# Performance work log

Measured on AMD Instinct MI355X. Metric: run time of the kernel, lower is better.

## Reference

```python
import jax, jax.numpy as jnp
import numpy as np

B, S, H, NH = 4, 1024, 1024, 16
HD = H // NH
I = 4096
EPS = 1e-12
BASE = 10000.0


def setup_inputs() -> dict:
    key = jax.random.key(0)
    ks = jax.random.split(key, 6)
    sc = 0.02
    return {
        "x": jax.random.normal(ks[0], (B, S, H), jnp.float32),
        "ln1_w": jnp.ones((H,), jnp.float32),
        "ln1_b": jnp.zeros((H,), jnp.float32),
        "qkv_w": jax.random.normal(ks[1], (3 * H, H), jnp.float32) * sc,
        "qkv_b": jnp.zeros((3 * H,), jnp.float32),
        "out_w": jax.random.normal(ks[2], (H, H), jnp.float32) * sc,
        "out_b": jnp.zeros((H,), jnp.float32),
        "ln2_w": jnp.ones((H,), jnp.float32),
        "ln2_b": jnp.zeros((H,), jnp.float32),
        "i2h_w": jax.random.normal(ks[3], (2 * I, H), jnp.float32) * sc,
        "i2h_b": jnp.zeros((2 * I,), jnp.float32),
        "h2o_w": jax.random.normal(ks[4], (H, I), jnp.float32) * sc,
        "h2o_b": jnp.zeros((H,), jnp.float32),
    }


def _layer_norm(x, w, b, eps=EPS):
    mu = jnp.mean(x, axis=-1, keepdims=True)
    var = jnp.mean(jnp.square(x - mu), axis=-1, keepdims=True)
    return (x - mu) * jax.lax.rsqrt(var + eps) * w + b


def _rope_cos_sin(seq_len, dim, base):
    # inv_freq = base ** linspace(0, -1 + 2/dim, dim//2), repeated twice
    half = jnp.power(base, jnp.linspace(0.0, -1.0 + 2.0 / dim, dim // 2, dtype=jnp.float32))
    inv_freq = jnp.concatenate([half, half])  # [dim]
    t = jnp.arange(seq_len, dtype=jnp.float32)
    freqs = t[:, None] * inv_freq[None, :]  # [seq, dim]
    return jnp.cos(freqs), jnp.sin(freqs)


def _rotate(x, cos, sin):
    # x: [B, NH, S, HD]; cos/sin: [S, HD]
    xl, xr = jnp.split(x, 2, axis=-1)
    x_rot = jnp.concatenate([-xr, xl], axis=-1)
    return x * cos + x_rot * sin


def _forward(x, ln1_w, ln1_b, qkv_w, qkv_b, out_w, out_b,
             ln2_w, ln2_b, i2h_w, i2h_b, h2o_w, h2o_b):
    b, s, h = x.shape
    # --- LeanSelfAttention (pre-LN, rotary, causal, residual) ---
    h_ln = _layer_norm(x, ln1_w, ln1_b)
    qkv = h_ln @ qkv_w.T + qkv_b  # [b, s, 3h]
    q, k, v = jnp.split(qkv, 3, axis=-1)
    to_heads = lambda t: t.reshape(b, s, NH, HD).transpose(0, 2, 1, 3)  # [b,nh,s,hd]
    q, k, v = to_heads(q), to_heads(k), to_heads(v)
    cos, sin = _rope_cos_sin(s, HD, BASE)
    q, k = _rotate(q, cos, sin), _rotate(k, cos, sin)
    scores = jnp.einsum("bhqd,bhkd->bhqk", q, k) / np.sqrt(HD).astype(np.float32)
    causal = jnp.tril(jnp.ones((s, s), dtype=bool))
    scores = jnp.where(causal, scores, jnp.float32(-10000.0))
    probs = jax.nn.softmax(scores, axis=-1)
    attn = jnp.einsum("bhqk,bhkd->bhqd", probs, v)
    attn = attn.transpose(0, 2, 1, 3).reshape(b, s, h)
    attn_out = attn @ out_w.T + out_b + x  # residual
    # --- LeanFFN (pre-LN, gated gelu, residual) ---
    ffn_ln = _layer_norm(attn_out, ln2_w, ln2_b)
    pre = ffn_ln @ i2h_w.T + i2h_b  # [b, s, 2I]
    gate, lin = jnp.split(pre, 2, axis=-1)
    hid = jax.nn.gelu(gate, approximate=False) * lin
    return hid @ h2o_w.T + h2o_b + attn_out


def reference(x, ln1_w, ln1_b, qkv_w, qkv_b, out_w, out_b,
              ln2_w, ln2_b, i2h_w, i2h_b, h2o_w, h2o_b):
    return _forward(x, ln1_w, ln1_b, qkv_w, qkv_b, out_w, out_b,
                    ln2_w, ln2_b, i2h_w, i2h_b, h2o_w, h2o_b)
```

## Files before the change

### kernel.cpp

```cpp
#include <hip/hip_runtime.h>
#include <cstdint>
#include <cstddef>

typedef __bf16 bf16;
typedef __bf16 bf16x4 __attribute__((ext_vector_type(4)));
typedef __bf16 bf16x8 __attribute__((ext_vector_type(8)));
typedef float  f32x4  __attribute__((ext_vector_type(4)));

#define GLD16(gptr, lptr)                                                      \
  __builtin_amdgcn_global_load_lds(                                            \
      (__attribute__((address_space(1))) unsigned int*)(gptr),                 \
      (__attribute__((address_space(3))) unsigned int*)(lptr), 16, 0, 0)

__global__ __launch_bounds__(256)
void convert_kernel(const float* __restrict__ src, bf16* __restrict__ dst, int n8)
{
    const int j = blockIdx.x * 256 + threadIdx.x;
    if (j >= n8) return;
    const float* s = src + (size_t)j * 8;
    bf16x8 o;
#pragma unroll
    for (int e = 0; e < 8; ++e) o[e] = (bf16)s[e];
    ((bf16x8*)dst)[j] = o;
}

template<class InT>
__global__ __launch_bounds__(256)
void ln_kernel(const InT* __restrict__ x, const float* __restrict__ w,
               const float* __restrict__ b, bf16* __restrict__ out)
{
    __shared__ float red[8];
    const int row = blockIdx.x;
    const int tid = threadIdx.x;
    const InT* xr = x + (size_t)row * 1024;
    float xf[4], s = 0.f, ss = 0.f;
#pragma unroll
    for (int j = 0; j < 4; ++j) {
        xf[j] = (float)xr[tid * 4 + j];
        s += xf[j]; ss += xf[j] * xf[j];
    }
#pragma unroll
    for (int off = 32; off > 0; off >>= 1) { s += __shfl_xor(s, off); ss += __shfl_xor(ss, off); }
    if ((tid & 63) == 0) { red[(tid >> 6) * 2] = s; red[(tid >> 6) * 2 + 1] = ss; }
    __syncthreads();
    s  = red[0] + red[2] + red[4] + red[6];
    ss = red[1] + red[3] + red[5] + red[7];
    const float mu   = s * (1.f / 1024.f);
    const float var  = ss * (1.f / 1024.f) - mu * mu;
    const float rstd = rsqrtf(var + 1e-12f);
    bf16x4 ov;
#pragma unroll
    for (int j = 0; j < 4; ++j)
        ov[j] = (bf16)((xf[j] - mu) * rstd * w[tid * 4 + j] + b[tid * 4 + j]);
    *(bf16x4*)(out + (size_t)row * 1024 + tid * 4) = ov;
}

template<int RES_MODE, bool OUT_F32>
__global__ __launch_bounds__(256)
void gemm_bt(const bf16* __restrict__ A, const bf16* __restrict__ W,
             const float* __restrict__ bias, const void* __restrict__ res,
             void* __restrict__ Cv, int M, int N, int K)
{
    __shared__ alignas(16) bf16 As[128][32];
    __shared__ alignas(16) bf16 Bs[128][32];
    const int tid  = threadIdx.x;
    const int lane = tid & 63, wid = tid >> 6;
    const int lr = lane & 15, lg = lane >> 4;
    const int kgrp = lg * 8;
    const int wm = (wid >> 1) * 64, wn = (wid & 1) * 64;
    const int row0 = blockIdx.x * 128, col0 = blockIdx.y * 128;

    f32x4 acc[4][4] = {};

    for (int k0 = 0; k0 < K; k0 += 32) {
#pragma unroll
        for (int i = 0; i < 2; ++i) {
            const int c = i * 256 + tid;
            const int r = c >> 2, k8 = (c & 3) * 8;
            GLD16(A + (size_t)(row0 + r) * K + k0 + k8,
                  (char*)&As[0][0] + (size_t)(i * 256 + wid * 64) * 16);
            GLD16(W + (size_t)(col0 + r) * K + k0 + k8,
                  (char*)&Bs[0][0] + (size_t)(i * 256 + wid * 64) * 16);
        }
        __syncthreads();
        bf16x8 af[4], bw[4];
#pragma unroll
        for (int mi = 0; mi < 4; ++mi) af[mi] = *(const bf16x8*)&As[wm + mi * 16 + lr][kgrp];
#pragma unroll
        for (int ni = 0; ni < 4; ++ni) bw[ni] = *(const bf16x8*)&Bs[wn + ni * 16 + lr][kgrp];
#pragma unroll
        for (int mi = 0; mi < 4; ++mi)
#pragma unroll
            for (int ni = 0; ni < 4; ++ni)
                acc[mi][ni] = __builtin_amdgcn_mfma_f32_16x16x32_bf16(
                    af[mi], bw[ni], acc[mi][ni], 0, 0, 0);
        __syncthreads();
    }

#pragma unroll
    for (int ni = 0; ni < 4; ++ni) {
        const int ccol = col0 + wn + ni * 16 + lr;
        const float bv = bias[ccol];
#pragma unroll
        for (int mi = 0; mi < 4; ++mi)
#pragma unroll
            for (int r = 0; r < 4; ++r) {
                const size_t crow = (size_t)(row0 + wm + mi * 16 + lg * 4 + r);
                float v = acc[mi][ni][r] + bv;
                if constexpr (RES_MODE == 1) v += ((const float*)res)[crow * N + ccol];
                if constexpr (RES_MODE == 2) v += (float)((const bf16*)res)[crow * N + ccol];
                if constexpr (OUT_F32) ((float*)Cv)[crow * N + ccol] = v;
                else                   ((bf16*)Cv)[crow * N + ccol] = (bf16)v;
            }
    }
}

__global__ __launch_bounds__(256)
void gemm_h2o_sk(const bf16* __restrict__ A, const bf16* __restrict__ W,
                 float* __restrict__ part)
{
    __shared__ alignas(16) bf16 As[128][32];
    __shared__ alignas(16) bf16 Bs[128][32];
    const int tid  = threadIdx.x;
    const int lane = tid & 63, wid = tid >> 6;
    const int lr = lane & 15, lg = lane >> 4;
    const int kgrp = lg * 8;
    const int wm = (wid >> 1) * 64, wn = (wid & 1) * 64;
    const int row0 = blockIdx.x * 128, col0 = blockIdx.y * 128;
    const int kbase = blockIdx.z * 1024;
    const int K = 4096;

    f32x4 acc[4][4] = {};

    for (int k0 = kbase; k0 < kbase + 1024; k0 += 32) {
#pragma unroll
        for (int i = 0; i < 2; ++i) {
            const int c = i * 256 + tid;
            const int r = c >> 2, k8 = (c & 3) * 8;
            GLD16(A + (size_t)(row0 + r) * K + k0 + k8,
                  (char*)&As[0][0] + (size_t)(i * 256 + wid * 64) * 16);
            GLD16(W + (size_t)(col0 + r) * K + k0 + k8,
                  (char*)&Bs[0][0] + (size_t)(i * 256 + wid * 64) * 16);
        }
        __syncthreads();
        bf16x8 af[4], bw[4];
#pragma unroll
        for (int mi = 0; mi < 4; ++mi) af[mi] = *(const bf16x8*)&As[wm + mi * 16 + lr][kgrp];
#pragma unroll
        for (int ni = 0; ni < 4; ++ni) bw[ni] = *(const bf16x8*)&Bs[wn + ni * 16 + lr][kgrp];
#pragma unroll
        for (int mi = 0; mi < 4; ++mi)
#pragma unroll
            for (int ni = 0; ni < 4; ++ni)
                acc[mi][ni] = __builtin_amdgcn_mfma_f32_16x16x32_bf16(
                    af[mi], bw[ni], acc[mi][ni], 0, 0, 0);
        __syncthreads();
    }

    float* dst = part + (size_t)blockIdx.z * 4096 * 1024;
#pragma unroll
    for (int ni = 0; ni < 4; ++ni) {
        const int ccol = col0 + wn + ni * 16 + lr;
#pragma unroll
        for (int mi = 0; mi < 4; ++mi)
#pragma unroll
            for (int r = 0; r < 4; ++r) {
                const size_t crow = (size_t)(row0 + wm + mi * 16 + lg * 4 + r);
                dst[crow * 1024 + ccol] = acc[mi][ni][r];
            }
    }
}

__global__ __launch_bounds__(256)
void h2o_reduce(const float* __restrict__ part, const float* __restrict__ bias,
                const bf16* __restrict__ res, float* __restrict__ out)
{
    const size_t g = ((size_t)blockIdx.x * 256 + threadIdx.x) * 4;
    const int col = (int)(g & 1023);
    f32x4 v = *(const f32x4*)(part + g);
#pragma unroll
    for (int s = 1; s < 4; ++s) {
        const f32x4 p = *(const f32x4*)(part + (size_t)s * 4096 * 1024 + g);
#pragma unroll
        for (int j = 0; j < 4; ++j) v[j] += p[j];
    }
    const f32x4 bv = *(const f32x4*)(bias + col);
    const bf16x4 rv = *(const bf16x4*)(res + g);
    f32x4 o;
#pragma unroll
    for (int j = 0; j < 4; ++j) o[j] = v[j] + bv[j] + (float)rv[j];
    *(f32x4*)(out + g) = o;
}

__global__ __launch_bounds__(256)
void gemm_qkv_rope(const bf16* __restrict__ A, const bf16* __restrict__ W,
                   const float* __restrict__ bias, bf16* __restrict__ q_r,
                   bf16* __restrict__ k_r, bf16* __restrict__ v_r)
{
    __shared__ alignas(16) bf16 As[128][32];
    __shared__ alignas(16) bf16 Bs[128][32];
    const int tid  = threadIdx.x;
    const int lane = tid & 63, wid = tid >> 6;
    const int lr = lane & 15, lg = lane >> 4;
    const int kgrp = lg * 8;
    const int wm = (wid >> 1) * 64, wn = (wid & 1) * 64;
    const int row0 = blockIdx.x * 128, col0 = blockIdx.y * 128;
    const int K = 1024;

    f32x4 acc[4][4] = {};

    for (int k0 = 0; k0 < K; k0 += 32) {
#pragma unroll
        for (int i = 0; i < 2; ++i) {
            const int c = i * 256 + tid;
            const int r = c >> 2, k8 = (c & 3) * 8;
            GLD16(A + (size_t)(row0 + r) * K + k0 + k8,
                  (char*)&As[0][0] + (size_t)(i * 256 + wid * 64) * 16);
            GLD16(W + (size_t)(col0 + r) * K + k0 + k8,
                  (char*)&Bs[0][0] + (size_t)(i * 256 + wid * 64) * 16);
        }
        __syncthreads();
        bf16x8 af[4], bw[4];
#pragma unroll
        for (int mi = 0; mi < 4; ++mi) af[mi] = *(const bf16x8*)&As[wm + mi * 16 + lr][kgrp];
#pragma unroll
        for (int ni = 0; ni < 4; ++ni) bw[ni] = *(const bf16x8*)&Bs[wn + ni * 16 + lr][kgrp];
#pragma unroll
        for (int mi = 0; mi < 4; ++mi)
#pragma unroll
            for (int ni = 0; ni < 4; ++ni)
                acc[mi][ni] = __builtin_amdgcn_mfma_f32_16x16x32_bf16(
                    af[mi], bw[ni], acc[mi][ni], 0, 0, 0);
        __syncthreads();
    }

    const int third = blockIdx.y >> 3;
    bf16* dst = (third == 0) ? q_r : (third == 1) ? k_r : v_r;
    const float qs = (third == 0) ? 0.125f : 1.f;
#pragma unroll
    for (int ni = 0; ni < 2; ++ni) {
        const int i_ = ni * 16 + lr;
        const int ccol = col0 + wn + ni * 16 + lr;
        const int h = (ccol >> 6) & 15;
        const float blo = bias[ccol], bhi = bias[ccol + 32];
        const float inv = __expf((float)i_ * (-9.210340371976184f / 32.f));
#pragma unroll
        for (int mi = 0; mi < 4; ++mi)
#pragma unroll
            for (int r = 0; r < 4; ++r) {
                const int crow = row0 + wm + mi * 16 + lg * 4 + r;
                const int s = crow & 1023, b = crow >> 10;
                const float lo = acc[mi][ni][r] + blo;
                const float hi = acc[mi][ni + 2][r] + bhi;
                const size_t ob = ((size_t)(b * 16 + h) * 1024 + s) * 64;
                if (third == 2) {
                    dst[ob + i_]      = (bf16)lo;
                    dst[ob + i_ + 32] = (bf16)hi;
                } else {
                    float sn, c;
                    sincosf((float)s * inv, &sn, &c);
                    dst[ob + i_]      = (bf16)((lo * c - hi * sn) * qs);
                    dst[ob + i_ + 32] = (bf16)((hi * c + lo * sn) * qs);
                }
            }
    }
}

__global__ __launch_bounds__(512, 2)
void gemm_i2h_g8(const bf16* __restrict__ A, const bf16* __restrict__ W,
                 const float* __restrict__ bias, bf16* __restrict__ hid)
{
    __shared__ alignas(16) char smem[3 * 32768];
    const int tid  = threadIdx.x;
    const int lane = tid & 63, wid = tid >> 6;
    const int lrr  = lane & 15, lg = lane >> 4;
    const int wr = wid >> 2, wc = wid & 3;
    const int row0 = blockIdx.x * 256;
    const int colh = blockIdx.y * 128 + wc * 32;
    const int NT = 32;

    const int cA0 = tid, cA1 = 512 + tid;
    const int rA0 = cA0 >> 2, rA1 = cA1 >> 2, rB = tid >> 2;
    const int swA0 = (((cA0 & 3) * 16) ^ (((rA0 >> 1) & 3) << 4)) >> 1;
    const int swA1 = (((cA1 & 3) * 16) ^ (((rA1 >> 1) & 3) << 4)) >> 1;
    const int swB  = (((tid & 3) * 16) ^ (((rB  >> 1) & 3) << 4)) >> 1;
    const bf16* gA0 = A + (size_t)(row0 + rA0) * 1024 + swA0;
    const bf16* gA1 = A + (size_t)(row0 + rA1) * 1024 + swA1;
    const bf16* gBg = W + (size_t)(blockIdx.y * 128 + rB) * 1024 + swB;
    const bf16* gBl = W + (size_t)(4096 + blockIdx.y * 128 + rB) * 1024 + swB;
    const int dA0 = (wid * 64) * 16, dA1 = (512 + wid * 64) * 16, dB = (wid * 64) * 16;

    f32x4 acc[8][4] = {};

    {
        char* b0 = smem;
        GLD16(gBg, b0 + 16384 + dB); GLD16(gBl, b0 + 24576 + dB);
        GLD16(gA0, b0 + dA0);        GLD16(gA1, b0 + dA1);
        char* b1 = smem + 32768;
        GLD16(gBg + 32, b1 + 16384 + dB); GLD16(gBl + 32, b1 + 24576 + dB);
        GLD16(gA0 + 32, b1 + dA0);        GLD16(gA1 + 32, b1 + dA1);
    }
    asm volatile("s_waitcnt vmcnt(4)\ns_barrier" ::: "memory");

    int cur = 0, stg = 2;
    for (int t = 0; t < NT; ++t) {
        const char* bA  = smem + cur * 32768;
        const char* bBg = bA + 16384;
        const char* bBl = bA + 24576;
        char* sB = smem + stg * 32768;
        const int k0s = (t + 2) * 32;
        const bool dostg = (t < NT - 2);

        if (dostg) { GLD16(gBg + k0s, sB + 16384 + dB); GLD16(gBl + k0s, sB + 24576 + dB); }
        bf16x8 bf[4], af[4];
        const int bcol = lg * 16;
#pragma unroll
        for (int nv = 0; nv < 4; ++nv) {
            const int row = wc * 32 + (nv & 1) * 16 + lrr;
            const char* base = (nv < 2) ? bBg : bBl;
            bf[nv] = *(const bf16x8*)(base + row * 64 + (bcol ^ (((row >> 1) & 3) << 4)));
        }
#pragma unroll
        for (int mi = 0; mi < 4; ++mi) {
            const int row = wr * 128 + mi * 16 + lrr;
            af[mi] = *(const bf16x8*)(bA + row * 64 + (bcol ^ (((row >> 1) & 3) << 4)));
        }
        __builtin_amdgcn_s_barrier();
        __builtin_amdgcn_s_setprio(1);
#pragma unroll
        for (int mi = 0; mi < 4; ++mi)
#pragma unroll
            for (int nv = 0; nv < 4; ++nv)
                acc[mi][nv] = __builtin_amdgcn_mfma_f32_16x16x32_bf16(
                    af[mi], bf[nv], acc[mi][nv], 0, 0, 0);
        __builtin_amdgcn_s_setprio(0);
        __builtin_amdgcn_s_barrier();

        if (dostg) { GLD16(gA0 + k0s, sB + dA0); GLD16(gA1 + k0s, sB + dA1); }
#pragma unroll
        for (int mi = 0; mi < 4; ++mi) {
            const int row = wr * 128 + (4 + mi) * 16 + lrr;
            af[mi] = *(const bf16x8*)(bA + row * 64 + (bcol ^ (((row >> 1) & 3) << 4)));
        }
        __builtin_amdgcn_s_barrier();
        __builtin_amdgcn_s_setprio(1);
#pragma unroll
        for (int mi = 0; mi < 4; ++mi)
#pragma unroll
            for (int nv = 0; nv < 4; ++nv)
                acc[4 + mi][nv] = __builtin_amdgcn_mfma_f32_16x16x32_bf16(
                    af[mi], bf[nv], acc[4 + mi][nv], 0, 0, 0);
        __builtin_amdgcn_s_setprio(0);

        if (dostg) asm volatile("s_waitcnt vmcnt(4)\ns_barrier" ::: "memory");
        else       asm volatile("s_waitcnt vmcnt(0)\ns_barrier" ::: "memory");
        cur = (cur == 2) ? 0 : cur + 1;
        stg = (stg == 2) ? 0 : stg + 1;
    }

#pragma unroll
    for (int c = 0; c < 2; ++c) {
        const int gcol = colh + c * 16 + lrr;
        const float bg_ = bias[gcol], bl_ = bias[4096 + gcol];
#pragma unroll
        for (int mi = 0; mi < 8; ++mi)
#pragma unroll
            for (int r = 0; r < 4; ++r) {
                const size_t row = (size_t)(row0 + wr * 128 + mi * 16 + lg * 4 + r);
                const float g = acc[mi][c][r] + bg_;
                const float l = acc[mi][2 + c][r] + bl_;
                const float ge = 0.5f * g * (1.f + erff(g * 0.70710678118654752f));
                hid[row * 4096 + gcol] = (bf16)(ge * l);
            }
    }
}

__global__ __launch_bounds__(256)
void attn_kernel(const bf16* __restrict__ q_r, const bf16* __restrict__ k_r,
                 const bf16* __restrict__ v_r, bf16* __restrict__ attn)
{
    __shared__ alignas(16) bf16 Ks[64][72];
    __shared__ alignas(16) bf16 Vt[64][72];
    __shared__ alignas(16) bf16 Ps[4][16][72];
    const int qt = blockIdx.x, bh = blockIdx.y;
    const int tid = threadIdx.x, lane = tid & 63, w = tid >> 6;
    const int lr = lane & 15, lg = lane >> 4;
    const int kgrp = lg * 8;
    const int qbase = qt * 64;

    const bf16* qrow = q_r + ((size_t)bh * 1024 + qbase + w * 16 + lr) * 64;
    const bf16x8 qf0 = *(const bf16x8*)(qrow + kgrp);
    const bf16x8 qf1 = *(const bf16x8*)(qrow + 32 + kgrp);

    f32x4 o[4] = {};
    float m_r[4], l_r[4];
#pragma unroll
    for (int r = 0; r < 4; ++r) { m_r[r] = -1e30f; l_r[r] = 0.f; }

    const int nchunk = qt + 1;
    for (int ic = 0; ic < nchunk; ++ic) {
        const int kb = ic * 64;
        __syncthreads();
#pragma unroll
        for (int i = 0; i < 2; ++i) {
            const int c = i * 256 + tid;
            const int row = c >> 3, e8 = (c & 7) * 8;
            *(bf16x8*)&Ks[row][e8] =
                *(const bf16x8*)(k_r + ((size_t)bh * 1024 + kb + row) * 64 + e8);
            const bf16x8 vv =
                *(const bf16x8*)(v_r + ((size_t)bh * 1024 + kb + row) * 64 + e8);
#pragma unroll
            for (int j = 0; j < 8; ++j) Vt[e8 + j][row] = vv[j];
        }
        __syncthreads();

        f32x4 sv[4] = {};
#pragma unroll
        for (int nb = 0; nb < 4; ++nb) {
            const bf16x8 kf0 = *(const bf16x8*)&Ks[nb * 16 + lr][kgrp];
            const bf16x8 kf1 = *(const bf16x8*)&Ks[nb * 16 + lr][32 + kgrp];
            sv[nb] = __builtin_amdgcn_mfma_f32_16x16x32_bf16(qf0, kf0, sv[nb], 0, 0, 0);
            sv[nb] = __builtin_amdgcn_mfma_f32_16x16x32_bf16(qf1, kf1, sv[nb], 0, 0, 0);
        }

        const bool diag = (kb == qbase);
        float pv[4][4];
#pragma unroll
        for (int r = 0; r < 4; ++r) {
            float s0[4];
#pragma unroll
            for (int nb = 0; nb < 4; ++nb) {
                float t = sv[nb][r];
                if (diag && (nb * 16 + lr) > (w * 16 + lg * 4 + r)) t = -10000.f;
                s0[nb] = t;
            }
            float rm = fmaxf(fmaxf(s0[0], s0[1]), fmaxf(s0[2], s0[3]));
#pragma unroll
            for (int off = 1; off < 16; off <<= 1) rm = fmaxf(rm, __shfl_xor(rm, off));
            const float nm = fmaxf(m_r[r], rm);
            const float sc = __expf(m_r[r] - nm);
            float rs = 0.f;
#pragma unroll
            for (int nb = 0; nb < 4; ++nb) {
                const float p = __expf(s0[nb] - nm);
                pv[nb][r] = p; rs += p;
            }
#pragma unroll
            for (int off = 1; off < 16; off <<= 1) rs += __shfl_xor(rs, off);
            l_r[r] = l_r[r] * sc + rs;
            m_r[r] = nm;
#pragma unroll
            for (int nb = 0; nb < 4; ++nb) o[nb][r] *= sc;
        }

#pragma unroll
        for (int nb = 0; nb < 4; ++nb)
#pragma unroll
            for (int r = 0; r < 4; ++r)
                Ps[w][lg * 4 + r][nb * 16 + lr] = (bf16)pv[nb][r];
#pragma unroll
        for (int nb = 0; nb < 4; ++nb)
#pragma unroll
            for (int ks = 0; ks < 2; ++ks) {
                const bf16x8 pa = *(const bf16x8*)&Ps[w][lr][ks * 32 + kgrp];
                const bf16x8 vb = *(const bf16x8*)&Vt[nb * 16 + lr][ks * 32 + kgrp];
                o[nb] = __builtin_amdgcn_mfma_f32_16x16x32_bf16(pa, vb, o[nb], 0, 0, 0);
            }
    }

    const int b = bh >> 4, head = bh & 15;
#pragma unroll
    for (int nb = 0; nb < 4; ++nb)
#pragma unroll
        for (int r = 0; r < 4; ++r) {
            const size_t rw = (size_t)(b * 1024 + qbase + w * 16 + lg * 4 + r);
            attn[rw * 1024 + head * 64 + nb * 16 + lr] = (bf16)(o[nb][r] / l_r[r]);
        }
}

extern "C" void kernel_launch(void* const* d_in, const int* in_sizes, int n_in,
                              void* d_out, int out_size, void* d_ws, size_t ws_size,
                              hipStream_t stream)
{
    const float* x    = (const float*)d_in[0];
    const float* ln1w = (const float*)d_in[1];
    const float* ln1b = (const float*)d_in[2];
    const float* qkvw = (const float*)d_in[3];
    const float* qkvb = (const float*)d_in[4];
    const float* outw = (const float*)d_in[5];
    const float* outb = (const float*)d_in[6];
    const float* ln2w = (const float*)d_in[7];
    const float* ln2b = (const float*)d_in[8];
    const float* i2hw = (const float*)d_in[9];
    const float* i2hb = (const float*)d_in[10];
    const float* h2ow = (const float*)d_in[11];
    const float* h2ob = (const float*)d_in[12];

    char* ws = (char*)d_ws;
    const size_t MB = 1024 * 1024;

    bf16*  h_ln    = (bf16*)(ws + 0);
    bf16*  q_r     = (bf16*)(ws + 8 * MB);
    bf16*  k_r     = (bf16*)(ws + 16 * MB);
    bf16*  v_r     = (bf16*)(ws + 24 * MB);
    bf16*  attn    = (bf16*)(ws + 32 * MB);
    bf16*  ffnln   = (bf16*)(ws + 40 * MB);
    float* part    = (float*)(ws + 0);
    bf16*  attnout = (bf16*)(ws + 64 * MB);
    bf16*  hid     = (bf16*)(ws + 72 * MB);
    bf16*  qkvw_c  = (bf16*)(ws + 104 * MB);
    bf16*  outw_c  = (bf16*)(ws + 110 * MB);
    bf16*  i2hw_c  = (bf16*)(ws + 112 * MB);
    bf16*  h2ow_c  = (bf16*)(ws + 128 * MB);

    convert_kernel<<<1536, 256, 0, stream>>>(qkvw, qkvw_c, 3145728 / 8);
    convert_kernel<<< 512, 256, 0, stream>>>(outw, outw_c, 1048576 / 8);
    convert_kernel<<<4096, 256, 0, stream>>>(i2hw, i2hw_c, 8388608 / 8);
    convert_kernel<<<2048, 256, 0, stream>>>(h2ow, h2ow_c, 4194304 / 8);

    ln_kernel<float><<<4096, 256, 0, stream>>>(x, ln1w, ln1b, h_ln);
    gemm_qkv_rope<<<dim3(32, 24), 256, 0, stream>>>(h_ln, qkvw_c, qkvb,
                                                    q_r, k_r, v_r);
    attn_kernel<<<dim3(16, 64), 256, 0, stream>>>(q_r, k_r, v_r, attn);
    gemm_bt<1, false><<<dim3(32, 8), 256, 0, stream>>>(
        attn, outw_c, outb, x, attnout, 4096, 1024, 1024);
    ln_kernel<bf16><<<4096, 256, 0, stream>>>(attnout, ln2w, ln2b, ffnln);
    gemm_i2h_g8<<<dim3(16, 32), 512, 0, stream>>>(ffnln, i2hw_c, i2hb, hid);
    gemm_h2o_sk<<<dim3(32, 8, 4), 256, 0, stream>>>(hid, h2ow_c, part);
    h2o_reduce<<<4096, 256, 0, stream>>>(part, h2ob, attnout, (float*)d_out);
}
```

Measured before the change: 473.1 us.

## Pair causal query tiles per block and swizzle transposed V in shared memory

The attention kernel now assigns each block two query tiles (p and 15-p) so every block does the same amount of causal work, and the K/V chunks loaded into shared memory are reused by both tiles. The transposed V buffer uses an XOR swizzle to reduce bank conflicts on its transposed writes. K and V fragments are hoisted into registers once per chunk. The grid halves to 512 blocks, which lowers parallelism and raises register pressure from two sets of accumulators.

```diff
diff --git a/kernel.cpp b/kernel.cpp
--- a/kernel.cpp
+++ b/kernel.cpp
@@ -380,25 +380,30 @@
                  const bf16* __restrict__ v_r, bf16* __restrict__ attn)
 {
     __shared__ alignas(16) bf16 Ks[64][72];
-    __shared__ alignas(16) bf16 Vt[64][72];
+    __shared__ alignas(16) bf16 Vt[64 * 72];
     __shared__ alignas(16) bf16 Ps[4][16][72];
-    const int qt = blockIdx.x, bh = blockIdx.y;
+    const int p = blockIdx.x, bh = blockIdx.y;
     const int tid = threadIdx.x, lane = tid & 63, w = tid >> 6;
     const int lr = lane & 15, lg = lane >> 4;
     const int kgrp = lg * 8;
-    const int qbase = qt * 64;
-
-    const bf16* qrow = q_r + ((size_t)bh * 1024 + qbase + w * 16 + lr) * 64;
-    const bf16x8 qf0 = *(const bf16x8*)(qrow + kgrp);
-    const bf16x8 qf1 = *(const bf16x8*)(qrow + 32 + kgrp);
-
-    f32x4 o[4] = {};
-    float m_r[4], l_r[4];
-#pragma unroll
-    for (int r = 0; r < 4; ++r) { m_r[r] = -1e30f; l_r[r] = 0.f; }
-
-    const int nchunk = qt + 1;
-    for (int ic = 0; ic < nchunk; ++ic) {
+    const int qt_hi = 15 - p, qt_lo = p;
+    const int qbh = qt_hi * 64, qbl = qt_lo * 64;
+
+    const bf16* qrowh = q_r + ((size_t)bh * 1024 + qbh + w * 16 + lr) * 64;
+    const bf16x8 qh0 = *(const bf16x8*)(qrowh + kgrp);
+    const bf16x8 qh1 = *(const bf16x8*)(qrowh + 32 + kgrp);
+    const bf16* qrowl = q_r + ((size_t)bh * 1024 + qbl + w * 16 + lr) * 64;
+    const bf16x8 ql0 = *(const bf16x8*)(qrowl + kgrp);
+    const bf16x8 ql1 = *(const bf16x8*)(qrowl + 32 + kgrp);
+
+    f32x4 oh[4] = {}, ol[4] = {};
+    float mh[4], lh[4], ml[4], ll[4];
+#pragma unroll
+    for (int r = 0; r < 4; ++r) { mh[r] = -1e30f; lh[r] = 0.f; ml[r] = -1e30f; ll[r] = 0.f; }
+
+    const int myrow = w * 16 + lg * 4;
+
+    for (int ic = 0; ic <= qt_hi; ++ic) {
         const int kb = ic * 64;
         __syncthreads();
 #pragma unroll
@@ -409,73 +414,105 @@
                 *(const bf16x8*)(k_r + ((size_t)bh * 1024 + kb + row) * 64 + e8);
             const bf16x8 vv =
                 *(const bf16x8*)(v_r + ((size_t)bh * 1024 + kb + row) * 64 + e8);
-#pragma unroll
-            for (int j = 0; j < 8; ++j) Vt[e8 + j][row] = vv[j];
-        }
-        __syncthreads();
-
-        f32x4 sv[4] = {};
+            const int s8 = row >> 3, s7 = row & 7;
+#pragma unroll
+            for (int j = 0; j < 8; ++j) {
+                const int d = e8 + j;
+                Vt[d * 72 + ((s8 ^ (d >> 3)) << 3) + s7] = vv[j];
+            }
+        }
+        __syncthreads();
+
+        bf16x8 kf0[4], kf1[4];
 #pragma unroll
         for (int nb = 0; nb < 4; ++nb) {
-            const bf16x8 kf0 = *(const bf16x8*)&Ks[nb * 16 + lr][kgrp];
-            const bf16x8 kf1 = *(const bf16x8*)&Ks[nb * 16 + lr][32 + kgrp];
-            sv[nb] = __builtin_amdgcn_mfma_f32_16x16x32_bf16(qf0, kf0, sv[nb], 0, 0, 0);
-            sv[nb] = __builtin_amdgcn_mfma_f32_16x16x32_bf16(qf1, kf1, sv[nb], 0, 0, 0);
-        }
-
-        const bool diag = (kb == qbase);
-        float pv[4][4];
-#pragma unroll
-        for (int r = 0; r < 4; ++r) {
-            float s0[4];
+            kf0[nb] = *(const bf16x8*)&Ks[nb * 16 + lr][kgrp];
+            kf1[nb] = *(const bf16x8*)&Ks[nb * 16 + lr][32 + kgrp];
+        }
+        bf16x8 vf[4][2];
+#pragma unroll
+        for (int nb = 0; nb < 4; ++nb) {
+            const int d = nb * 16 + lr, dh = d >> 3;
+#pragma unroll
+            for (int ks = 0; ks < 2; ++ks)
+                vf[nb][ks] = *(const bf16x8*)&Vt[d * 72 + (((ks * 4 + lg) ^ dh) << 3)];
+        }
+
+#pragma unroll
+        for (int half = 0; half < 2; ++half) {
+            if (half == 1 && ic > qt_lo) break;
+            const bf16x8 qf0 = half ? ql0 : qh0;
+            const bf16x8 qf1 = half ? ql1 : qh1;
+            const bool diag = half ? (ic == qt_lo) : (ic == qt_hi);
+            float* m_r = half ? ml : mh;
+            float* l_r = half ? ll : lh;
+            f32x4* o = half ? ol : oh;
+
+            f32x4 sv[4] = {};
 #pragma unroll
             for (int nb = 0; nb < 4; ++nb) {
-                float t = sv[nb][r];
-                if (diag && (nb * 16 + lr) > (w * 16 + lg * 4 + r)) t = -10000.f;
-                s0[nb] = t;
-            }
-            float rm = fmaxf(fmaxf(s0[0], s0[1]), fmaxf(s0[2], s0[3]));
-#pragma unroll
-            for (int off = 1; off < 16; off <<= 1) rm = fmaxf(rm, __shfl_xor(rm, off));
-            const float nm = fmaxf(m_r[r], rm);
-            const float sc = __expf(m_r[r] - nm);
-            float rs = 0.f;
-#pragma unroll
-            for (int nb = 0; nb < 4; ++nb) {
-                const float p = __expf(s0[nb] - nm);
-                pv[nb][r] = p; rs += p;
-            }
-#pragma unroll
-            for (int off = 1; off < 16; off <<= 1) rs += __shfl_xor(rs, off);
-            l_r[r] = l_r[r] * sc + rs;
-            m_r[r] = nm;
-#pragma unroll
-            for (int nb = 0; nb < 4; ++nb) o[nb][r] *= sc;
-        }
-
+                sv[nb] = __builtin_amdgcn_mfma_f32_16x16x32_bf16(qf0, kf0[nb], sv[nb], 0, 0, 0);
+                sv[nb] = __builtin_amdgcn_mfma_f32_16x16x32_bf16(qf1, kf1[nb], sv[nb], 0, 0, 0);
+            }
+
+            float pv[4][4];
+#pragma unroll
+            for (int r = 0; r < 4; ++r) {
+                float s0[4];
+#pragma unroll
+                for (int nb = 0; nb < 4; ++nb) {
+                    float t = sv[nb][r];
+                    if (diag && (nb * 16 + lr) > (myrow + r)) t = -10000.f;
+                    s0[nb] = t;
+                }
+                float rm = fmaxf(fmaxf(s0[0], s0[1]), fmaxf(s0[2], s0[3]));
+#pragma unroll
+                for (int off = 1; off < 16; off <<= 1) rm = fmaxf(rm, __shfl_xor(rm, off));
+                const float nm = fmaxf(m_r[r], rm);
+                const float sc = __expf(m_r[r] - nm);
+                float rs = 0.f;
+#pragma unroll
+                for (int nb = 0; nb < 4; ++nb) {
+                    const float pe = __expf(s0[nb] - nm);
+                    pv[nb][r] = pe; rs += pe;
+                }
+#pragma unroll
+                for (int off = 1; off < 16; off <<= 1) rs += __shfl_xor(rs, off);
+                l_r[r] = l_r[r] * sc + rs;
+                m_r[r] = nm;
+#pragma unroll
+                for (int nb = 0; nb < 4; ++nb) o[nb][r] *= sc;
+            }
+
+#pragma unroll
+            for (int nb = 0; nb < 4; ++nb)
+#pragma unroll
+                for (int r = 0; r < 4; ++r)
+                    Ps[w][lg * 4 + r][nb * 16 + lr] = (bf16)pv[nb][r];
+#pragma unroll
+            for (int nb = 0; nb < 4; ++nb)
+#pragma unroll
+                for (int ks = 0; ks < 2; ++ks) {
+                    const bf16x8 pa = *(const bf16x8*)&Ps[w][lr][ks * 32 + kgrp];
+                    o[nb] = __builtin_amdgcn_mfma_f32_16x16x32_bf16(pa, vf[nb][ks], o[nb], 0, 0, 0);
+                }
+        }
+    }
+
+    const int b = bh >> 4, head = bh & 15;
+#pragma unroll
+    for (int half = 0; half < 2; ++half) {
+        const int qb = half ? qbl : qbh;
+        const f32x4* o = half ? ol : oh;
+        const float* l_r = half ? ll : lh;
 #pragma unroll
         for (int nb = 0; nb < 4; ++nb)
 #pragma unroll
-            for (int r = 0; r < 4; ++r)
-                Ps[w][lg * 4 + r][nb * 16 + lr] = (bf16)pv[nb][r];
-#pragma unroll
-        for (int nb = 0; nb < 4; ++nb)
-#pragma unroll
-            for (int ks = 0; ks < 2; ++ks) {
-                const bf16x8 pa = *(const bf16x8*)&Ps[w][lr][ks * 32 + kgrp];
-                const bf16x8 vb = *(const bf16x8*)&Vt[nb * 16 + lr][ks * 32 + kgrp];
-                o[nb] = __builtin_amdgcn_mfma_f32_16x16x32_bf16(pa, vb, o[nb], 0, 0, 0);
-            }
-    }
-
-    const int b = bh >> 4, head = bh & 15;
-#pragma unroll
-    for (int nb = 0; nb < 4; ++nb)
-#pragma unroll
-        for (int r = 0; r < 4; ++r) {
-            const size_t rw = (size_t)(b * 1024 + qbase + w * 16 + lg * 4 + r);
-            attn[rw * 1024 + head * 64 + nb * 16 + lr] = (bf16)(o[nb][r] / l_r[r]);
-        }
+            for (int r = 0; r < 4; ++r) {
+                const size_t rw = (size_t)(b * 1024 + qb + myrow + r);
+                attn[rw * 1024 + head * 64 + nb * 16 + lr] = (bf16)(o[nb][r] / l_r[r]);
+            }
+    }
 }
 
 extern "C" void kernel_launch(void* const* d_in, const int* in_sizes, int n_in,
@@ -521,7 +558,7 @@
     ln_kernel<float><<<4096, 256, 0, stream>>>(x, ln1w, ln1b, h_ln);
     gemm_qkv_rope<<<dim3(32, 24), 256, 0, stream>>>(h_ln, qkvw_c, qkvb,
                                                     q_r, k_r, v_r);
-    attn_kernel<<<dim3(16, 64), 256, 0, stream>>>(q_r, k_r, v_r, attn);
+    attn_kernel<<<dim3(8, 64), 256, 0, stream>>>(q_r, k_r, v_r, attn);
     gemm_bt<1, false><<<dim3(32, 8), 256, 0, stream>>>(
         attn, outw_c, outb, x, attnout, 4096, 1024, 1024);
     ln_kernel<bf16><<<4096, 256, 0, stream>>>(attnout, ln2w, ln2b, ffnln);
```

After: 442.8 us. 1.07x faster.
